# Kernel optimization log

Hardware: AMD Instinct MI355X
Metric: run time of the kernel (lower is better)

## Reference

```python
import jax, jax.numpy as jnp
import numpy as np

N = 8192
H = 512
E = 262144
NUM_LAYERS = 2
LAYER_DECAY = 0.4
INIT_W = 1e-05


def setup_inputs() -> dict:
    key = jax.random.key(0)
    ks = jax.random.split(key, 6)
    x = jax.random.normal(ks[0], (N, H), dtype=jnp.float32)
    rows = jax.random.randint(ks[1], (E,), 0, N, dtype=jnp.int32)
    cols = jax.random.randint(ks[2], (E,), 0, N, dtype=jnp.int32)
    vals = jax.random.uniform(ks[3], (E,), dtype=jnp.float32)
    # near-identity init as in GSS_GNNLayer (torch Linear: y = x @ W.T + b)
    W1 = jax.random.normal(ks[4], (H, H), dtype=jnp.float32) * INIT_W + jnp.eye(H, dtype=jnp.float32)
    b1 = jnp.zeros((H,), dtype=jnp.float32)
    W2 = jax.random.normal(ks[5], (H, H), dtype=jnp.float32) * INIT_W + jnp.eye(H, dtype=jnp.float32)
    b2 = jnp.zeros((H,), dtype=jnp.float32)
    return {"x": x, "rows": rows, "cols": cols, "vals": vals,
            "W1": W1, "b1": b1, "W2": W2, "b2": b2}


def _spmm(rows, cols, vals, dense):
    # sparse [N,N] @ dense [N,H] via gather + segment-sum scatter-add
    return jax.ops.segment_sum(vals[:, None] * dense[cols], rows, num_segments=N)


def _gcn_layer(x, rows, cols, vals, W1, b1, W2, b2):
    Ax = _spmm(rows, cols, vals, x)                      # [N,H]
    pre1 = Ax @ W1.T + b1
    Ax_x = _spmm(rows, cols, vals, Ax * x)               # A(Ax * x)
    pre2 = Ax_x @ W2.T + b2
    pre = pre1 + pre2
    return pre, jax.nn.elu(pre)


def reference(x, rows, cols, vals, W1, b1, W2, b2):
    residual = None
    for _ in range(NUM_LAYERS):  # shared weights across layers, as in source
        pre, x = _gcn_layer(x, rows, cols, vals, W1, b1, W2, b2)
        if residual is not None:
            x = residual + LAYER_DECAY * x
        residual = pre
    # decoder: row-wise L2 normalize (eps=1e-12 like F.normalize), dense gram, relu
    norm = jnp.maximum(jnp.linalg.norm(x, axis=1, keepdims=True), 1e-12)
    hidden_emb = x / norm
    adj_preds = jax.nn.relu(hidden_emb @ hidden_emb.T)   # [N,N]
    return adj_preds, hidden_emb
```

## Files before the change

kernel.cpp:

```cpp
#include <hip/hip_runtime.h>

#define N_NODES 8192
#define HDIM    512
#define NEDGE   262144

typedef __attribute__((ext_vector_type(8))) short bf16x8;
typedef __attribute__((ext_vector_type(4))) float f32x4;

__device__ inline unsigned short f2bf(float f) {
  unsigned u = __float_as_uint(f);
  unsigned r = (u + 0x7FFFu + ((u >> 16) & 1u)) >> 16;
  return (unsigned short)r;
}
__device__ inline float bf2f(short s) {
  return __uint_as_float(((unsigned)(unsigned short)s) << 16);
}

__device__ inline void gload16(const void* g, void* l) {
  __builtin_amdgcn_global_load_lds(
      (const __attribute__((address_space(1))) unsigned*)g,
      (__attribute__((address_space(3))) unsigned*)l, 16, 0, 0);
}

__global__ void zero_kernel(int* __restrict__ p) {
  p[blockIdx.x * 256 + threadIdx.x] = 0;
}

__global__ void hist_kernel(const int* __restrict__ rows, int* __restrict__ counts) {
  int e = blockIdx.x * 256 + threadIdx.x;
  atomicAdd(&counts[rows[e]], 1);
}

__global__ __launch_bounds__(1024) void scan_kernel(const int* __restrict__ counts,
                                                    int* __restrict__ offs,
                                                    int* __restrict__ cursor) {
  __shared__ int s[1024];
  int tid = threadIdx.x;
  int local[8];
  int sum = 0;
#pragma unroll
  for (int i = 0; i < 8; ++i) { local[i] = counts[tid * 8 + i]; sum += local[i]; }
  s[tid] = sum;
  __syncthreads();
  for (int d = 1; d < 1024; d <<= 1) {
    int v = (tid >= d) ? s[tid - d] : 0;
    __syncthreads();
    s[tid] += v;
    __syncthreads();
  }
  int base = (tid > 0) ? s[tid - 1] : 0;
#pragma unroll
  for (int i = 0; i < 8; ++i) {
    offs[tid * 8 + i] = base;
    cursor[tid * 8 + i] = base;
    base += local[i];
  }
  if (tid == 1023) offs[8192] = base;
}

__global__ void scatter_kernel(const int* __restrict__ rows, const int* __restrict__ cols,
                               const float* __restrict__ vals, int* cursor,
                               int2* __restrict__ edges) {
  int e = blockIdx.x * 256 + threadIdx.x;
  int slot = atomicAdd(&cursor[rows[e]], 1);
  edges[slot] = make_int2(cols[e], __float_as_int(vals[e]));
}

template <int MODE>
__global__ __launch_bounds__(256) void spmm_bf(const int* __restrict__ offs,
                                               const int2* __restrict__ edges,
                                               const short* __restrict__ Xbf,
                                               const float* __restrict__ aux,
                                               short* __restrict__ outb,
                                               short* __restrict__ prodb) {
  int row = blockIdx.x * 4 + (threadIdx.x >> 6);
  int lane = threadIdx.x & 63;
  int h0 = lane * 8;
  float acc[8] = {0.f, 0.f, 0.f, 0.f, 0.f, 0.f, 0.f, 0.f};
  int e0 = offs[row], e1 = offs[row + 1];
  int p = e0;

  int2 ma0, ma1, ma2, ma3;
  bf16x8 xa0, xa1, xa2, xa3;

  if (p + 4 <= e1) {
    ma0 = edges[p]; ma1 = edges[p + 1]; ma2 = edges[p + 2]; ma3 = edges[p + 3];
    xa0 = *reinterpret_cast<const bf16x8*>(Xbf + (size_t)ma0.x * HDIM + h0);
    xa1 = *reinterpret_cast<const bf16x8*>(Xbf + (size_t)ma1.x * HDIM + h0);
    xa2 = *reinterpret_cast<const bf16x8*>(Xbf + (size_t)ma2.x * HDIM + h0);
    xa3 = *reinterpret_cast<const bf16x8*>(Xbf + (size_t)ma3.x * HDIM + h0);
    p += 4;
    for (; p + 4 <= e1; p += 4) {
      int2 mb0 = edges[p], mb1 = edges[p + 1], mb2 = edges[p + 2], mb3 = edges[p + 3];
      bf16x8 xb0 = *reinterpret_cast<const bf16x8*>(Xbf + (size_t)mb0.x * HDIM + h0);
      bf16x8 xb1 = *reinterpret_cast<const bf16x8*>(Xbf + (size_t)mb1.x * HDIM + h0);
      bf16x8 xb2 = *reinterpret_cast<const bf16x8*>(Xbf + (size_t)mb2.x * HDIM + h0);
      bf16x8 xb3 = *reinterpret_cast<const bf16x8*>(Xbf + (size_t)mb3.x * HDIM + h0);
      float v0 = __int_as_float(ma0.y), v1 = __int_as_float(ma1.y);
      float v2 = __int_as_float(ma2.y), v3 = __int_as_float(ma3.y);
#pragma unroll
      for (int j = 0; j < 8; ++j) {
        acc[j] = fmaf(v0, bf2f(xa0[j]), acc[j]);
        acc[j] = fmaf(v1, bf2f(xa1[j]), acc[j]);
        acc[j] = fmaf(v2, bf2f(xa2[j]), acc[j]);
        acc[j] = fmaf(v3, bf2f(xa3[j]), acc[j]);
      }
      ma0 = mb0; ma1 = mb1; ma2 = mb2; ma3 = mb3;
      xa0 = xb0; xa1 = xb1; xa2 = xb2; xa3 = xb3;
    }
    {
      float v0 = __int_as_float(ma0.y), v1 = __int_as_float(ma1.y);
      float v2 = __int_as_float(ma2.y), v3 = __int_as_float(ma3.y);
#pragma unroll
      for (int j = 0; j < 8; ++j) {
        acc[j] = fmaf(v0, bf2f(xa0[j]), acc[j]);
        acc[j] = fmaf(v1, bf2f(xa1[j]), acc[j]);
        acc[j] = fmaf(v2, bf2f(xa2[j]), acc[j]);
        acc[j] = fmaf(v3, bf2f(xa3[j]), acc[j]);
      }
    }
  }
  for (; p < e1; ++p) {
    int2 e = edges[p];
    float v = __int_as_float(e.y);
    bf16x8 xr = *reinterpret_cast<const bf16x8*>(Xbf + (size_t)e.x * HDIM + h0);
#pragma unroll
    for (int j = 0; j < 8; ++j) acc[j] = fmaf(v, bf2f(xr[j]), acc[j]);
  }

  bf16x8 o;
#pragma unroll
  for (int j = 0; j < 8; ++j) o[j] = (short)f2bf(acc[j]);
  *reinterpret_cast<bf16x8*>(outb + (size_t)row * 1024 + h0) = o;
  if (MODE != 2) {
    const float4* ap = reinterpret_cast<const float4*>(aux + (size_t)row * HDIM + h0);
    float4 a0 = ap[0], a1 = ap[1];
    float xv[8] = {a0.x, a0.y, a0.z, a0.w, a1.x, a1.y, a1.z, a1.w};
    if (MODE == 1) {
#pragma unroll
      for (int j = 0; j < 8; ++j) xv[j] = xv[j] > 0.f ? xv[j] : expm1f(xv[j]);
    }
    bf16x8 t;
#pragma unroll
    for (int j = 0; j < 8; ++j) t[j] = (short)f2bf(acc[j] * xv[j]);
    *reinterpret_cast<bf16x8*>(prodb + (size_t)row * HDIM + h0) = t;
  }
}

__device__ inline void cast8(const float* src, short* dst) {
  const float4* p = reinterpret_cast<const float4*>(src);
  float4 a = p[0], b = p[1];
  bf16x8 o;
  o[0] = (short)f2bf(a.x); o[1] = (short)f2bf(a.y);
  o[2] = (short)f2bf(a.z); o[3] = (short)f2bf(a.w);
  o[4] = (short)f2bf(b.x); o[5] = (short)f2bf(b.y);
  o[6] = (short)f2bf(b.z); o[7] = (short)f2bf(b.w);
  *reinterpret_cast<bf16x8*>(dst) = o;
}

__global__ void prep_kernel(const float* __restrict__ x,
                            const float* __restrict__ W1, const float* __restrict__ W2,
                            const float* __restrict__ b1, const float* __restrict__ b2,
                            short* __restrict__ Xbf, short* __restrict__ Bbuf,
                            float* __restrict__ b12) {
  int b = blockIdx.x;
  if (b < 2048) {
    int t = b * 256 + threadIdx.x;
    int row = t >> 6, c0 = (t & 63) * 8;
    cast8(x + (size_t)row * 512 + c0, Xbf + (size_t)row * 512 + c0);
  } else if (b < 2176) {
    int t = (b - 2048) * 256 + threadIdx.x;
    int row = t >> 6, c0 = (t & 63) * 8;
    cast8(W1 + (size_t)row * 512 + c0, Bbuf + (size_t)row * 1024 + c0);
  } else if (b < 2304) {
    int t = (b - 2176) * 256 + threadIdx.x;
    int row = t >> 6, c0 = (t & 63) * 8;
    cast8(W2 + (size_t)row * 512 + c0, Bbuf + (size_t)row * 1024 + 512 + c0);
  } else {
    int j = threadIdx.x;
    b12[j] = b1[j] + b2[j];
    b12[j + 256] = b1[j + 256] + b2[j + 256];
  }
}

__global__ __launch_bounds__(256) void rownorm_kernel(const float* __restrict__ X,
                                                      float* __restrict__ outf,
                                                      short* __restrict__ outb) {
  int row = blockIdx.x * 4 + (threadIdx.x >> 6);
  int lane = threadIdx.x & 63;
  int h0 = lane * 8;
  const float4* p = reinterpret_cast<const float4*>(X + (size_t)row * HDIM + h0);
  float4 a = p[0], b = p[1];
  float s = a.x * a.x + a.y * a.y + a.z * a.z + a.w * a.w +
            b.x * b.x + b.y * b.y + b.z * b.z + b.w * b.w;
#pragma unroll
  for (int off = 1; off < 64; off <<= 1) s += __shfl_xor(s, off, 64);
  float inv = 1.f / fmaxf(sqrtf(s), 1e-12f);
  a.x *= inv; a.y *= inv; a.z *= inv; a.w *= inv;
  b.x *= inv; b.y *= inv; b.z *= inv; b.w *= inv;
  float4* q = reinterpret_cast<float4*>(outf + (size_t)row * HDIM + h0);
  q[0] = a; q[1] = b;
  bf16x8 o;
  o[0] = (short)f2bf(a.x); o[1] = (short)f2bf(a.y);
  o[2] = (short)f2bf(a.z); o[3] = (short)f2bf(a.w);
  o[4] = (short)f2bf(b.x); o[5] = (short)f2bf(b.y);
  o[6] = (short)f2bf(b.z); o[7] = (short)f2bf(b.w);
  *reinterpret_cast<bf16x8*>(outb + (size_t)row * HDIM + h0) = o;
}

template <int MODE>
__global__ __launch_bounds__(256) void gemm_lds(const short* __restrict__ A,
                                                const short* __restrict__ B,
                                                int N, int K, int nbn,
                                                const float* __restrict__ bias,
                                                const float* __restrict__ resid,
                                                float* __restrict__ out0,
                                                short* __restrict__ out1bf) {
  __shared__ __align__(16) short la[128 * 64];
  __shared__ __align__(16) short lb[128 * 64];

  int q = gridDim.x >> 3;
  int id = (blockIdx.x & 7) * q + (blockIdx.x >> 3);
  int bn, bm;
  if (MODE == 2) {
    int sid = id >> 6, wid = id & 63;
    int srow = sid >> 3, scol = sid & 7;
    bm = (srow * 8 + (wid >> 3)) * 128;
    bn = (scol * 8 + (wid & 7)) * 128;
  } else {
    bn = (id % nbn) * 128;
    bm = (id / nbn) * 128;
  }

  int lane = threadIdx.x & 63;
  int wave = threadIdx.x >> 6;

  int rsub = lane >> 3;
  int csrc = (lane & 7) ^ rsub;
  size_t ldkB = (size_t)K * 2;
  const char* gA0 = (const char*)A + (size_t)(bm + wave * 32 + rsub) * ldkB + csrc * 16;
  const char* gB0 = (const char*)B + (size_t)(bn + wave * 32 + rsub) * ldkB + csrc * 16;
  char* lA0 = (char*)la + wave * 4096;
  char* lB0 = (char*)lb + wave * 4096;

  f32x4 zero = {0.f, 0.f, 0.f, 0.f};
  f32x4 acc[4][4];
#pragma unroll
  for (int m = 0; m < 4; ++m)
#pragma unroll
    for (int n = 0; n < 4; ++n) acc[m][n] = zero;

  int rlo = lane & 15;
  int khi = lane >> 4;
  int wm = wave >> 1, wn = wave & 1;

  for (int k0 = 0; k0 < K; k0 += 64) {
    __syncthreads();
#pragma unroll
    for (int j = 0; j < 4; ++j) {
      gload16(gA0 + (size_t)j * 8 * ldkB + (size_t)k0 * 2, lA0 + j * 1024);
      gload16(gB0 + (size_t)j * 8 * ldkB + (size_t)k0 * 2, lB0 + j * 1024);
    }
    __syncthreads();
#pragma unroll
    for (int kk = 0; kk < 2; ++kk) {
      bf16x8 av[4], bv[4];
#pragma unroll
      for (int m = 0; m < 4; ++m) {
        int ra = wm * 64 + m * 16 + rlo;
        int pc = (kk * 4 + khi) ^ (ra & 7);
        av[m] = *reinterpret_cast<const bf16x8*>((const char*)la + ra * 128 + pc * 16);
      }
#pragma unroll
      for (int n = 0; n < 4; ++n) {
        int rb = wn * 64 + n * 16 + rlo;
        int pc = (kk * 4 + khi) ^ (rb & 7);
        bv[n] = *reinterpret_cast<const bf16x8*>((const char*)lb + rb * 128 + pc * 16);
      }
#pragma unroll
      for (int m = 0; m < 4; ++m)
#pragma unroll
        for (int n = 0; n < 4; ++n)
          acc[m][n] = __builtin_amdgcn_mfma_f32_16x16x32_bf16(av[m], bv[n], acc[m][n], 0, 0, 0);
    }
  }

  int obm = bm + wm * 64;
  int obn = bn + wn * 64;
  int crow = (lane >> 4) * 4;
  int ccol = lane & 15;
#pragma unroll
  for (int n = 0; n < 4; ++n) {
    int c = obn + n * 16 + ccol;
    float bc = (MODE == 2) ? 0.f : bias[c];
#pragma unroll
    for (int m = 0; m < 4; ++m) {
#pragma unroll
      for (int v = 0; v < 4; ++v) {
        int r = obm + m * 16 + crow + v;
        size_t idx = (size_t)r * N + c;
        float val = acc[m][n][v];
        if (MODE == 0) {
          float pvl = val + bc;
          out0[idx] = pvl;
          float e = pvl > 0.f ? pvl : expm1f(pvl);
          out1bf[idx] = (short)f2bf(e);
        } else if (MODE == 1) {
          float pvl = val + bc;
          out0[idx] = resid[idx] + 0.4f * (pvl > 0.f ? pvl : expm1f(pvl));
        } else {
          out0[idx] = val > 0.f ? val : 0.f;
        }
      }
    }
  }
}

extern "C" void kernel_launch(void* const* d_in, const int* in_sizes, int n_in,
                              void* d_out, int out_size, void* d_ws, size_t ws_size,
                              hipStream_t stream) {
  const float* x  = (const float*)d_in[0];
  const int* rows = (const int*)d_in[1];
  const int* cols = (const int*)d_in[2];
  const float* vals = (const float*)d_in[3];
  const float* W1 = (const float*)d_in[4];
  const float* b1 = (const float*)d_in[5];
  const float* W2 = (const float*)d_in[6];
  const float* b2 = (const float*)d_in[7];

  float* out_adj = (float*)d_out;
  float* out_hid = out_adj + (size_t)N_NODES * N_NODES;

  char* w = (char*)d_ws;
  size_t off = 0;
  auto alloc = [&](size_t bytes) -> void* {
    void* p = w + off;
    off += (bytes + 255) & ~(size_t)255;
    return p;
  };
  int* counts   = (int*)alloc(8192 * sizeof(int));
  int* offs     = (int*)alloc(8193 * sizeof(int));
  int* cursor   = (int*)alloc(8192 * sizeof(int));
  int2* edges   = (int2*)alloc((size_t)NEDGE * sizeof(int2));
  float* b12    = (float*)alloc(HDIM * sizeof(float));
  short* Xbf    = (short*)alloc((size_t)N_NODES * HDIM * sizeof(short));
  short* Tbf    = (short*)alloc((size_t)N_NODES * HDIM * sizeof(short));
  short* Abuf   = (short*)alloc((size_t)N_NODES * 1024 * sizeof(short));
  short* Bbuf   = (short*)alloc((size_t)512 * 1024 * sizeof(short));
  float* pre1   = (float*)alloc((size_t)N_NODES * HDIM * sizeof(float));
  float* Hf     = (float*)alloc((size_t)N_NODES * HDIM * sizeof(float));
  short* Hbuf   = (short*)alloc((size_t)N_NODES * HDIM * sizeof(short));

  zero_kernel<<<32, 256, 0, stream>>>(counts);
  hist_kernel<<<NEDGE / 256, 256, 0, stream>>>(rows, counts);
  scan_kernel<<<1, 1024, 0, stream>>>(counts, offs, cursor);
  scatter_kernel<<<NEDGE / 256, 256, 0, stream>>>(rows, cols, vals, cursor, edges);

  prep_kernel<<<2305, 256, 0, stream>>>(x, W1, W2, b1, b2, Xbf, Bbuf, b12);

  spmm_bf<0><<<2048, 256, 0, stream>>>(offs, edges, Xbf, x, Abuf, Tbf);
  spmm_bf<2><<<2048, 256, 0, stream>>>(offs, edges, Tbf, nullptr, Abuf + 512, nullptr);
  gemm_lds<0><<<256, 256, 0, stream>>>(Abuf, Bbuf, 512, 1024, 4, b12, nullptr, pre1, Xbf);

  spmm_bf<1><<<2048, 256, 0, stream>>>(offs, edges, Xbf, pre1, Abuf, Tbf);
  spmm_bf<2><<<2048, 256, 0, stream>>>(offs, edges, Tbf, nullptr, Abuf + 512, nullptr);
  gemm_lds<1><<<256, 256, 0, stream>>>(Abuf, Bbuf, 512, 1024, 4, b12, pre1, Hf, nullptr);

  rownorm_kernel<<<2048, 256, 0, stream>>>(Hf, out_hid, Hbuf);
  gemm_lds<2><<<4096, 256, 0, stream>>>(Hbuf, Hbuf, 8192, 512, 64, nullptr, nullptr, out_adj, nullptr);
}
```

Baseline: 328.2 us.

## Add 256x256-tile multistage gram kernel and deepen SpMM unrolling to 8 edges

Replaces the generic 128x128 GEMM used for the final 8192x8192 gram product with a dedicated 512-thread kernel. It uses 256x256 output tiles, a 4-slot LDS ring filled by global_load_lds two stages ahead, and explicit vmcnt waits and priority hints around the MFMA loop. The larger tile is meant to cut global/L2 traffic per output and hide load latency, but the unswizzled LDS layout risks bank conflicts, and the large accumulator set raises register pressure. Separately, the SpMM gather loop is unrolled from 4 to 8 edges in flight to expose more memory-level parallelism.

```diff
diff --git a/kernel.cpp b/kernel.cpp
--- a/kernel.cpp
+++ b/kernel.cpp
@@ -80,44 +80,37 @@
   int e0 = offs[row], e1 = offs[row + 1];
   int p = e0;
 
-  int2 ma0, ma1, ma2, ma3;
-  bf16x8 xa0, xa1, xa2, xa3;
-
-  if (p + 4 <= e1) {
-    ma0 = edges[p]; ma1 = edges[p + 1]; ma2 = edges[p + 2]; ma3 = edges[p + 3];
-    xa0 = *reinterpret_cast<const bf16x8*>(Xbf + (size_t)ma0.x * HDIM + h0);
-    xa1 = *reinterpret_cast<const bf16x8*>(Xbf + (size_t)ma1.x * HDIM + h0);
-    xa2 = *reinterpret_cast<const bf16x8*>(Xbf + (size_t)ma2.x * HDIM + h0);
-    xa3 = *reinterpret_cast<const bf16x8*>(Xbf + (size_t)ma3.x * HDIM + h0);
-    p += 4;
-    for (; p + 4 <= e1; p += 4) {
-      int2 mb0 = edges[p], mb1 = edges[p + 1], mb2 = edges[p + 2], mb3 = edges[p + 3];
-      bf16x8 xb0 = *reinterpret_cast<const bf16x8*>(Xbf + (size_t)mb0.x * HDIM + h0);
-      bf16x8 xb1 = *reinterpret_cast<const bf16x8*>(Xbf + (size_t)mb1.x * HDIM + h0);
-      bf16x8 xb2 = *reinterpret_cast<const bf16x8*>(Xbf + (size_t)mb2.x * HDIM + h0);
-      bf16x8 xb3 = *reinterpret_cast<const bf16x8*>(Xbf + (size_t)mb3.x * HDIM + h0);
-      float v0 = __int_as_float(ma0.y), v1 = __int_as_float(ma1.y);
-      float v2 = __int_as_float(ma2.y), v3 = __int_as_float(ma3.y);
-#pragma unroll
-      for (int j = 0; j < 8; ++j) {
-        acc[j] = fmaf(v0, bf2f(xa0[j]), acc[j]);
-        acc[j] = fmaf(v1, bf2f(xa1[j]), acc[j]);
-        acc[j] = fmaf(v2, bf2f(xa2[j]), acc[j]);
-        acc[j] = fmaf(v3, bf2f(xa3[j]), acc[j]);
+  int2 ma[8];
+  bf16x8 xa[8];
+  if (p + 8 <= e1) {
+#pragma unroll
+    for (int u = 0; u < 8; ++u) ma[u] = edges[p + u];
+#pragma unroll
+    for (int u = 0; u < 8; ++u)
+      xa[u] = *reinterpret_cast<const bf16x8*>(Xbf + (size_t)ma[u].x * HDIM + h0);
+    p += 8;
+    for (; p + 8 <= e1; p += 8) {
+      int2 mb[8];
+      bf16x8 xb[8];
+#pragma unroll
+      for (int u = 0; u < 8; ++u) mb[u] = edges[p + u];
+#pragma unroll
+      for (int u = 0; u < 8; ++u)
+        xb[u] = *reinterpret_cast<const bf16x8*>(Xbf + (size_t)mb[u].x * HDIM + h0);
+#pragma unroll
+      for (int u = 0; u < 8; ++u) {
+        float v = __int_as_float(ma[u].y);
+#pragma unroll
+        for (int j = 0; j < 8; ++j) acc[j] = fmaf(v, bf2f(xa[u][j]), acc[j]);
       }
-      ma0 = mb0; ma1 = mb1; ma2 = mb2; ma3 = mb3;
-      xa0 = xb0; xa1 = xb1; xa2 = xb2; xa3 = xb3;
-    }
-    {
-      float v0 = __int_as_float(ma0.y), v1 = __int_as_float(ma1.y);
-      float v2 = __int_as_float(ma2.y), v3 = __int_as_float(ma3.y);
-#pragma unroll
-      for (int j = 0; j < 8; ++j) {
-        acc[j] = fmaf(v0, bf2f(xa0[j]), acc[j]);
-        acc[j] = fmaf(v1, bf2f(xa1[j]), acc[j]);
-        acc[j] = fmaf(v2, bf2f(xa2[j]), acc[j]);
-        acc[j] = fmaf(v3, bf2f(xa3[j]), acc[j]);
-      }
+#pragma unroll
+      for (int u = 0; u < 8; ++u) { ma[u] = mb[u]; xa[u] = xb[u]; }
+    }
+#pragma unroll
+    for (int u = 0; u < 8; ++u) {
+      float v = __int_as_float(ma[u].y);
+#pragma unroll
+      for (int j = 0; j < 8; ++j) acc[j] = fmaf(v, bf2f(xa[u][j]), acc[j]);
     }
   }
   for (; p < e1; ++p) {
@@ -221,16 +214,8 @@
 
   int q = gridDim.x >> 3;
   int id = (blockIdx.x & 7) * q + (blockIdx.x >> 3);
-  int bn, bm;
-  if (MODE == 2) {
-    int sid = id >> 6, wid = id & 63;
-    int srow = sid >> 3, scol = sid & 7;
-    bm = (srow * 8 + (wid >> 3)) * 128;
-    bn = (scol * 8 + (wid & 7)) * 128;
-  } else {
-    bn = (id % nbn) * 128;
-    bm = (id / nbn) * 128;
-  }
+  int bn = (id % nbn) * 128;
+  int bm = (id / nbn) * 128;
 
   int lane = threadIdx.x & 63;
   int wave = threadIdx.x >> 6;
@@ -292,7 +277,7 @@
 #pragma unroll
   for (int n = 0; n < 4; ++n) {
     int c = obn + n * 16 + ccol;
-    float bc = (MODE == 2) ? 0.f : bias[c];
+    float bc = bias[c];
 #pragma unroll
     for (int m = 0; m < 4; ++m) {
 #pragma unroll
@@ -305,12 +290,103 @@
           out0[idx] = pvl;
           float e = pvl > 0.f ? pvl : expm1f(pvl);
           out1bf[idx] = (short)f2bf(e);
-        } else if (MODE == 1) {
+        } else {
           float pvl = val + bc;
           out0[idx] = resid[idx] + 0.4f * (pvl > 0.f ? pvl : expm1f(pvl));
-        } else {
-          out0[idx] = val > 0.f ? val : 0.f;
         }
+      }
+    }
+  }
+}
+
+__device__ inline void wait_vmcnt_u(int n) {
+  if (n == 8)      asm volatile("s_waitcnt vmcnt(8)" ::: "memory");
+  else if (n == 4) asm volatile("s_waitcnt vmcnt(4)" ::: "memory");
+  else             asm volatile("s_waitcnt vmcnt(0)" ::: "memory");
+}
+
+__global__ __launch_bounds__(512, 2) void gram256(const short* __restrict__ H,
+                                                  float* __restrict__ out) {
+  __shared__ __align__(16) char lds[4 * 32768];
+  const int NK = HDIM / 32;
+
+  int id = (blockIdx.x & 7) * 128 + (blockIdx.x >> 3);
+  int sid = id >> 6, wt = id & 63;
+  int bm = ((sid >> 2) * 8 + (wt >> 3)) * 256;
+  int bn = ((sid & 3) * 8 + (wt & 7)) * 256;
+
+  int tid = threadIdx.x;
+  int wid = tid >> 6;
+  int lane = tid & 63;
+  int wr = wid >> 2;
+  int wc = wid & 3;
+  int rlo = lane & 15;
+  int khi = lane >> 4;
+  int wbase = wid * 1024;
+
+  const char* Ab = (const char*)H + (size_t)bm * 1024;
+  const char* Bb = (const char*)H + (size_t)bn * 1024;
+  int r4 = tid >> 2, c4 = tid & 3;
+
+  f32x4 zero = {0.f, 0.f, 0.f, 0.f};
+  f32x4 acc[8][4];
+#pragma unroll
+  for (int m = 0; m < 8; ++m)
+#pragma unroll
+    for (int n = 0; n < 4; ++n) acc[m][n] = zero;
+
+  auto stage = [&](int s) {
+    char* slot = lds + ((s & 3) << 15);
+    size_t go = (size_t)s * 64 + c4 * 16;
+    gload16(Ab + (size_t)r4 * 1024 + go,          slot + wbase);
+    gload16(Ab + (size_t)(r4 + 128) * 1024 + go,  slot + 8192 + wbase);
+    gload16(Bb + (size_t)r4 * 1024 + go,          slot + 16384 + wbase);
+    gload16(Bb + (size_t)(r4 + 128) * 1024 + go,  slot + 24576 + wbase);
+  };
+
+  stage(0);
+  stage(1);
+
+  for (int s = 0; s < NK; ++s) {
+    if (s + 2 < NK) stage(s + 2);
+    int out_cnt = 4 * ((s + 1 < NK) + (s + 2 < NK));
+    wait_vmcnt_u(out_cnt);
+    __builtin_amdgcn_s_barrier();
+    __builtin_amdgcn_sched_barrier(0);
+
+    const char* slot = lds + ((s & 3) << 15);
+    bf16x8 av[8], bv[4];
+#pragma unroll
+    for (int m = 0; m < 8; ++m)
+      av[m] = *reinterpret_cast<const bf16x8*>(
+          slot + (wr * 128 + m * 16 + rlo) * 64 + khi * 16);
+#pragma unroll
+    for (int n = 0; n < 4; ++n)
+      bv[n] = *reinterpret_cast<const bf16x8*>(
+          slot + 16384 + (wc * 64 + n * 16 + rlo) * 64 + khi * 16);
+
+    __builtin_amdgcn_s_setprio(1);
+#pragma unroll
+    for (int m = 0; m < 8; ++m)
+#pragma unroll
+      for (int n = 0; n < 4; ++n)
+        acc[m][n] = __builtin_amdgcn_mfma_f32_16x16x32_bf16(av[m], bv[n], acc[m][n], 0, 0, 0);
+    __builtin_amdgcn_s_setprio(0);
+  }
+
+  int obm = bm + wr * 128;
+  int obn = bn + wc * 64;
+  int crow = khi * 4;
+#pragma unroll
+  for (int m = 0; m < 8; ++m) {
+#pragma unroll
+    for (int n = 0; n < 4; ++n) {
+      int c = obn + n * 16 + rlo;
+#pragma unroll
+      for (int v = 0; v < 4; ++v) {
+        int r = obm + m * 16 + crow + v;
+        float val = acc[m][n][v];
+        out[(size_t)r * N_NODES + c] = val > 0.f ? val : 0.f;
       }
     }
   }
@@ -367,5 +443,5 @@
   gemm_lds<1><<<256, 256, 0, stream>>>(Abuf, Bbuf, 512, 1024, 4, b12, pre1, Hf, nullptr);
 
   rownorm_kernel<<<2048, 256, 0, stream>>>(Hf, out_hid, Hbuf);
-  gemm_lds<2><<<4096, 256, 0, stream>>>(Hbuf, Hbuf, 8192, 512, 64, nullptr, nullptr, out_adj, nullptr);
-}
+  gram256<<<1024, 512, 0, stream>>>(Hbuf, out_adj);
+}
```

Result: slower. 347.9 us (+6.0%).

## Replace gram GEMM with 128x256-tile triple-buffered kernel and memset counts

Applied to the files above, without the earlier changes.

Adds a dedicated gram-matrix kernel for the final H·Hᵀ ReLU product. It uses 128x256 output tiles with 512 threads, triple-buffered direct-to-LDS loads and MFMA priority hints, in place of the generic 128x128 gemm_lds path. The goal is more reuse per tile and overlap of global loads with MFMA work in the dominant 8192x8192 output stage. The zero kernel is also replaced by hipMemsetAsync. The new LDS layout is unswizzled, so bank conflicts are possible.

```diff
diff --git a/kernel.cpp b/kernel.cpp
--- a/kernel.cpp
+++ b/kernel.cpp
@@ -5,6 +5,7 @@
 #define NEDGE   262144
 
 typedef __attribute__((ext_vector_type(8))) short bf16x8;
+typedef __attribute__((ext_vector_type(4))) short bf16x4;
 typedef __attribute__((ext_vector_type(4))) float f32x4;
 
 __device__ inline unsigned short f2bf(float f) {
@@ -20,10 +21,6 @@
   __builtin_amdgcn_global_load_lds(
       (const __attribute__((address_space(1))) unsigned*)g,
       (__attribute__((address_space(3))) unsigned*)l, 16, 0, 0);
-}
-
-__global__ void zero_kernel(int* __restrict__ p) {
-  p[blockIdx.x * 256 + threadIdx.x] = 0;
 }
 
 __global__ void hist_kernel(const int* __restrict__ rows, int* __restrict__ counts) {
@@ -221,16 +218,8 @@
 
   int q = gridDim.x >> 3;
   int id = (blockIdx.x & 7) * q + (blockIdx.x >> 3);
-  int bn, bm;
-  if (MODE == 2) {
-    int sid = id >> 6, wid = id & 63;
-    int srow = sid >> 3, scol = sid & 7;
-    bm = (srow * 8 + (wid >> 3)) * 128;
-    bn = (scol * 8 + (wid & 7)) * 128;
-  } else {
-    bn = (id % nbn) * 128;
-    bm = (id / nbn) * 128;
-  }
+  int bn = (id % nbn) * 128;
+  int bm = (id / nbn) * 128;
 
   int lane = threadIdx.x & 63;
   int wave = threadIdx.x >> 6;
@@ -292,7 +281,7 @@
 #pragma unroll
   for (int n = 0; n < 4; ++n) {
     int c = obn + n * 16 + ccol;
-    float bc = (MODE == 2) ? 0.f : bias[c];
+    float bc = bias[c];
 #pragma unroll
     for (int m = 0; m < 4; ++m) {
 #pragma unroll
@@ -305,12 +294,98 @@
           out0[idx] = pvl;
           float e = pvl > 0.f ? pvl : expm1f(pvl);
           out1bf[idx] = (short)f2bf(e);
-        } else if (MODE == 1) {
+        } else {
           float pvl = val + bc;
           out0[idx] = resid[idx] + 0.4f * (pvl > 0.f ? pvl : expm1f(pvl));
-        } else {
-          out0[idx] = val > 0.f ? val : 0.f;
         }
+      }
+    }
+  }
+}
+
+__global__ __launch_bounds__(512, 4) void gram256(const short* __restrict__ H,
+                                                  float* __restrict__ out) {
+  __shared__ __align__(16) char lds[3 * 24576];
+  const int NK = HDIM / 32;
+
+  int id = (blockIdx.x & 7) * 256 + (blockIdx.x >> 3);
+  int st = id >> 4, wt = id & 15;
+  int bm = ((st >> 3) * 4 + (wt >> 2)) * 128;
+  int bn = ((st & 7) * 4 + (wt & 3)) * 256;
+
+  int tid = threadIdx.x;
+  int wid = tid >> 6;
+  int lane = tid & 63;
+  int wr = wid >> 2;
+  int wc = wid & 3;
+  int rlo = lane & 15;
+  int khi = lane >> 4;
+  int wbase = wid * 1024;
+
+  const char* Ab = (const char*)H + (size_t)bm * 1024;
+  const char* Bb = (const char*)H + (size_t)bn * 1024;
+  int r4 = tid >> 2, c4 = tid & 3;
+
+  f32x4 zero = {0.f, 0.f, 0.f, 0.f};
+  f32x4 acc[4][4];
+#pragma unroll
+  for (int m = 0; m < 4; ++m)
+#pragma unroll
+    for (int n = 0; n < 4; ++n) acc[m][n] = zero;
+
+  auto stage = [&](int s) {
+    char* slot = lds + (s % 3) * 24576;
+    size_t go = (size_t)s * 64 + c4 * 16;
+    gload16(Ab + (size_t)r4 * 1024 + go,         slot + wbase);
+    gload16(Bb + (size_t)r4 * 1024 + go,         slot + 8192 + wbase);
+    gload16(Bb + (size_t)(r4 + 128) * 1024 + go, slot + 16384 + wbase);
+  };
+
+  stage(0);
+
+  for (int s = 0; s < NK; ++s) {
+    if (s + 1 < NK) {
+      stage(s + 1);
+      asm volatile("s_waitcnt vmcnt(3)" ::: "memory");
+    } else {
+      asm volatile("s_waitcnt vmcnt(0)" ::: "memory");
+    }
+    __builtin_amdgcn_s_barrier();
+    __builtin_amdgcn_sched_barrier(0);
+
+    const char* slot = lds + (s % 3) * 24576;
+    bf16x8 av[4], bv[4];
+#pragma unroll
+    for (int m = 0; m < 4; ++m)
+      av[m] = *reinterpret_cast<const bf16x8*>(
+          slot + (wr * 64 + m * 16 + rlo) * 64 + khi * 16);
+#pragma unroll
+    for (int n = 0; n < 4; ++n)
+      bv[n] = *reinterpret_cast<const bf16x8*>(
+          slot + 8192 + (wc * 64 + n * 16 + rlo) * 64 + khi * 16);
+
+    __builtin_amdgcn_s_setprio(1);
+#pragma unroll
+    for (int m = 0; m < 4; ++m)
+#pragma unroll
+      for (int n = 0; n < 4; ++n)
+        acc[m][n] = __builtin_amdgcn_mfma_f32_16x16x32_bf16(av[m], bv[n], acc[m][n], 0, 0, 0);
+    __builtin_amdgcn_s_setprio(0);
+  }
+
+  int obm = bm + wr * 64;
+  int obn = bn + wc * 64;
+  int crow = khi * 4;
+#pragma unroll
+  for (int m = 0; m < 4; ++m) {
+#pragma unroll
+    for (int n = 0; n < 4; ++n) {
+      int c = obn + n * 16 + rlo;
+#pragma unroll
+      for (int v = 0; v < 4; ++v) {
+        int r = obm + m * 16 + crow + v;
+        float val = acc[m][n][v];
+        out[(size_t)r * N_NODES + c] = val > 0.f ? val : 0.f;
       }
     }
   }
@@ -351,7 +426,7 @@
   float* Hf     = (float*)alloc((size_t)N_NODES * HDIM * sizeof(float));
   short* Hbuf   = (short*)alloc((size_t)N_NODES * HDIM * sizeof(short));
 
-  zero_kernel<<<32, 256, 0, stream>>>(counts);
+  hipMemsetAsync(counts, 0, 8192 * sizeof(int), stream);
   hist_kernel<<<NEDGE / 256, 256, 0, stream>>>(rows, counts);
   scan_kernel<<<1, 1024, 0, stream>>>(counts, offs, cursor);
   scatter_kernel<<<NEDGE / 256, 256, 0, stream>>>(rows, cols, vals, cursor, edges);
@@ -367,5 +442,5 @@
   gemm_lds<1><<<256, 256, 0, stream>>>(Abuf, Bbuf, 512, 1024, 4, b12, pre1, Hf, nullptr);
 
   rownorm_kernel<<<2048, 256, 0, stream>>>(Hf, out_hid, Hbuf);
-  gemm_lds<2><<<4096, 256, 0, stream>>>(Hbuf, Hbuf, 8192, 512, 64, nullptr, nullptr, out_adj, nullptr);
-}
+  gram256<<<2048, 512, 0, stream>>>(Hbuf, out_adj);
+}
```

Result: no change. 327.3 us (-0.3%).
